# Performance work log

Hardware: AMD Instinct MI355X
Metric: run time of the kernel (lower is better)

## Reference

```python
import jax, jax.numpy as jnp
import numpy as np

EPS = 1e-12  # F.normalize default eps
TEMPERATURE = 1.0


def _l2_normalize(x):
    n = jnp.sqrt(jnp.sum(x * x, axis=-1, keepdims=True))
    return x / jnp.maximum(n, EPS)


def setup_inputs() -> dict:
    key = jax.random.key(0)
    k1, k2 = jax.random.split(key)
    B, C, H, W = 16, 256, 128, 256
    K = 19
    features = jax.random.normal(k1, (B, C, H, W), dtype=jnp.float32)
    prototypes = jax.random.normal(k2, (K, C), dtype=jnp.float32)
    distance_scale = jnp.ones((1,), dtype=jnp.float32)
    return {"features": features, "prototypes": prototypes,
            "distance_scale": distance_scale}


def reference(features, prototypes, distance_scale):
    B, C, H, W = features.shape
    K = prototypes.shape[0]
    # [B,C,H,W] -> [B*H*W, C]
    x = features.transpose(0, 2, 3, 1).reshape(-1, C)
    xn = _l2_normalize(x)            # [N, C]
    pn = _l2_normalize(prototypes)   # [K, C]
    # pairwise Euclidean distance via the stable quadratic expansion
    # ||a-b||^2 = ||a||^2 + ||b||^2 - 2 a.b  (norms ~1 after normalization)
    xx = jnp.sum(xn * xn, axis=-1)   # [N]
    pp = jnp.sum(pn * pn, axis=-1)   # [K]
    d2 = xx[:, None] + pp[None, :] - 2.0 * jnp.einsum('nc,kc->nk', xn, pn)
    dist = jnp.sqrt(jnp.maximum(d2, 0.0))  # [N, K]
    dist = jnp.abs(distance_scale) * dist
    logits = -dist.reshape(B, H, W, K).transpose(0, 3, 1, 2)  # [B,K,H,W]
    return logits / TEMPERATURE
```

## Files before the change

### kernel.cpp

```cpp
#include <hip/hip_runtime.h>


namespace {
constexpr int kC   = 256;
constexpr int kK   = 19;
constexpr int kKP  = 20;
constexpr int kHW  = 128 * 256;
constexpr int kBlock = 256;
constexpr int kPixPerThread = 4;
}

__global__ __launch_bounds__(kBlock, 2)
void isomax_dist_kernel(const float* __restrict__ feat,
                        const float* __restrict__ proto,
                        const float* __restrict__ dscale,
                        float* __restrict__ out)
{
    __shared__ float pn_s[kC * kKP];
    __shared__ float pp_s[kK];

    const int tid  = threadIdx.x;
    const int lane = tid & 63;
    const int wv   = tid >> 6;

    for (int k = wv; k < kK; k += 4) {
        float v[4];
        float ss = 0.f;
        #pragma unroll
        for (int j = 0; j < 4; ++j) {
            v[j] = proto[k * kC + j * 64 + lane];
            ss = fmaf(v[j], v[j], ss);
        }
        #pragma unroll
        for (int m = 1; m < 64; m <<= 1)
            ss += __shfl_xor(ss, m, 64);
        const float nrm = sqrtf(ss);
        const float inv = 1.0f / fmaxf(nrm, 1e-12f);
        #pragma unroll
        for (int j = 0; j < 4; ++j)
            pn_s[(j * 64 + lane) * kKP + k] = v[j] * inv;
        if (lane == 0) pp_s[k] = ss * inv * inv;
    }
    __syncthreads();

    const int gpix = (blockIdx.x * kBlock + tid) * kPixPerThread;
    const int b    = gpix >> 15;
    const int hw   = gpix & (kHW - 1);
    const float* fp = feat + (size_t)b * kC * kHW + hw;

    float xx[4] = {0.f, 0.f, 0.f, 0.f};
    float4 dot[kK];
    #pragma unroll
    for (int k = 0; k < kK; ++k) dot[k] = make_float4(0.f, 0.f, 0.f, 0.f);

    for (int cc = 0; cc < kC; cc += 4) {
        float4 v[4];
        #pragma unroll
        for (int u = 0; u < 4; ++u)
            v[u] = *(const float4*)(fp + (size_t)(cc + u) * kHW);
        #pragma unroll
        for (int u = 0; u < 4; ++u) {
            const int c = cc + u;
            float4 P[5];
            const float4* row = (const float4*)(pn_s + c * kKP);
            #pragma unroll
            for (int q = 0; q < 5; ++q) P[q] = row[q];
            const float* p = (const float*)P;
            xx[0] = fmaf(v[u].x, v[u].x, xx[0]);
            xx[1] = fmaf(v[u].y, v[u].y, xx[1]);
            xx[2] = fmaf(v[u].z, v[u].z, xx[2]);
            xx[3] = fmaf(v[u].w, v[u].w, xx[3]);
            #pragma unroll
            for (int k = 0; k < kK; ++k) {
                dot[k].x = fmaf(p[k], v[u].x, dot[k].x);
                dot[k].y = fmaf(p[k], v[u].y, dot[k].y);
                dot[k].z = fmaf(p[k], v[u].z, dot[k].z);
                dot[k].w = fmaf(p[k], v[u].w, dot[k].w);
            }
        }
    }

    float inv[4], xnsq[4];
    #pragma unroll
    for (int j = 0; j < 4; ++j) {
        const float nrm = sqrtf(xx[j]);
        inv[j]  = 1.0f / fmaxf(nrm, 1e-12f);
        xnsq[j] = xx[j] * inv[j] * inv[j];
    }
    const float sc = fabsf(dscale[0]);

    float* op = out + (size_t)b * kK * kHW + hw;
    #pragma unroll
    for (int k = 0; k < kK; ++k) {
        const float ppk = pp_s[k];
        float4 o;
        o.x = -sc * sqrtf(fmaxf(xnsq[0] + ppk - 2.0f * dot[k].x * inv[0], 0.f));
        o.y = -sc * sqrtf(fmaxf(xnsq[1] + ppk - 2.0f * dot[k].y * inv[1], 0.f));
        o.z = -sc * sqrtf(fmaxf(xnsq[2] + ppk - 2.0f * dot[k].z * inv[2], 0.f));
        o.w = -sc * sqrtf(fmaxf(xnsq[3] + ppk - 2.0f * dot[k].w * inv[3], 0.f));
        *(float4*)(op + (size_t)k * kHW) = o;
    }
}

extern "C" void kernel_launch(void* const* d_in, const int* in_sizes, int n_in,
                              void* d_out, int out_size, void* d_ws, size_t ws_size,
                              hipStream_t stream) {
    const float* feat   = (const float*)d_in[0];
    const float* proto  = (const float*)d_in[1];
    const float* dscale = (const float*)d_in[2];
    float* out = (float*)d_out;

    const int npix    = in_sizes[0] / kC;
    const int threads = npix / kPixPerThread;
    const dim3 grid(threads / kBlock);
    isomax_dist_kernel<<<grid, kBlock, 0, stream>>>(feat, proto, dscale, out);
}
```

Before: 689.2 us.

## Precompute normalized prototypes in workspace and read via scalar constant loads

Prototype normalization moves into a separate single-block kernel that writes the padded normalized table and squared norms to workspace. The main kernel then reads prototype weights through address_space(4) constant pointers, which lets the compiler use scalar loads instead of per-block LDS staging and LDS reads. Pixels per thread drop from 4 to 2 and launch bounds rise to 4 blocks per SIMD, trading register reuse for occupancy. This adds an extra kernel launch and makes every thread issue its own uniform scalar loads of prototype data.

```diff
diff --git a/kernel.cpp b/kernel.cpp
--- a/kernel.cpp
+++ b/kernel.cpp
@@ -1,24 +1,23 @@
 #include <hip/hip_runtime.h>
+#include <stdint.h>
 
 
 namespace {
-constexpr int kC   = 256;
-constexpr int kK   = 19;
-constexpr int kKP  = 20;
-constexpr int kHW  = 128 * 256;
+constexpr int kC     = 256;
+constexpr int kK     = 19;
+constexpr int kKP    = 20;
+constexpr int kHW    = 128 * 256;
 constexpr int kBlock = 256;
-constexpr int kPixPerThread = 4;
+constexpr int kPix   = 2;
 }
 
-__global__ __launch_bounds__(kBlock, 2)
-void isomax_dist_kernel(const float* __restrict__ feat,
-                        const float* __restrict__ proto,
-                        const float* __restrict__ dscale,
-                        float* __restrict__ out)
+typedef __attribute__((address_space(4))) const float* cfp;
+
+__global__ void proto_prep(const float* __restrict__ proto,
+                           float* __restrict__ ws)
 {
-    __shared__ float pn_s[kC * kKP];
-    __shared__ float pp_s[kK];
-
+    float* pw = ws;
+    float* pp = ws + kC * kKP;
     const int tid  = threadIdx.x;
     const int lane = tid & 63;
     const int wv   = tid >> 6;
@@ -34,84 +33,90 @@
         #pragma unroll
         for (int m = 1; m < 64; m <<= 1)
             ss += __shfl_xor(ss, m, 64);
-        const float nrm = sqrtf(ss);
-        const float inv = 1.0f / fmaxf(nrm, 1e-12f);
+        const float inv = 1.0f / fmaxf(sqrtf(ss), 1e-12f);
         #pragma unroll
         for (int j = 0; j < 4; ++j)
-            pn_s[(j * 64 + lane) * kKP + k] = v[j] * inv;
-        if (lane == 0) pp_s[k] = ss * inv * inv;
+            pw[(j * 64 + lane) * kKP + k] = v[j] * inv;
+        if (lane == 0) pp[k] = ss * inv * inv;
     }
-    __syncthreads();
+    pw[tid * kKP + (kKP - 1)] = 0.f;
+}
 
-    const int gpix = (blockIdx.x * kBlock + tid) * kPixPerThread;
+__global__ __launch_bounds__(kBlock, 4)
+void isomax_main(const float* __restrict__ feat,
+                 const float* __restrict__ ws,
+                 const float* __restrict__ dscale,
+                 float* __restrict__ out)
+{
+    const int tid  = threadIdx.x;
+    const int gpix = (blockIdx.x * kBlock + tid) * kPix;
     const int b    = gpix >> 15;
     const int hw   = gpix & (kHW - 1);
-    const float* fp = feat + (size_t)b * kC * kHW + hw;
 
-    float xx[4] = {0.f, 0.f, 0.f, 0.f};
-    float4 dot[kK];
+    const float2* __restrict__ fp =
+        (const float2*)(feat + (size_t)b * kC * kHW + hw);
+
+    cfp pw = (cfp)(uintptr_t)ws;
+
+    float2 xx = make_float2(0.f, 0.f);
+    float2 dot[kK];
     #pragma unroll
-    for (int k = 0; k < kK; ++k) dot[k] = make_float4(0.f, 0.f, 0.f, 0.f);
+    for (int k = 0; k < kK; ++k) dot[k] = make_float2(0.f, 0.f);
 
     for (int cc = 0; cc < kC; cc += 4) {
-        float4 v[4];
+        float2 v[4];
         #pragma unroll
         for (int u = 0; u < 4; ++u)
-            v[u] = *(const float4*)(fp + (size_t)(cc + u) * kHW);
+            v[u] = fp[(size_t)(cc + u) * (kHW / 2)];
         #pragma unroll
         for (int u = 0; u < 4; ++u) {
             const int c = cc + u;
-            float4 P[5];
-            const float4* row = (const float4*)(pn_s + c * kKP);
+            float p[kKP];
             #pragma unroll
-            for (int q = 0; q < 5; ++q) P[q] = row[q];
-            const float* p = (const float*)P;
-            xx[0] = fmaf(v[u].x, v[u].x, xx[0]);
-            xx[1] = fmaf(v[u].y, v[u].y, xx[1]);
-            xx[2] = fmaf(v[u].z, v[u].z, xx[2]);
-            xx[3] = fmaf(v[u].w, v[u].w, xx[3]);
+            for (int q = 0; q < kKP; ++q)
+                p[q] = pw[c * kKP + q];
+            xx.x = fmaf(v[u].x, v[u].x, xx.x);
+            xx.y = fmaf(v[u].y, v[u].y, xx.y);
             #pragma unroll
             for (int k = 0; k < kK; ++k) {
                 dot[k].x = fmaf(p[k], v[u].x, dot[k].x);
                 dot[k].y = fmaf(p[k], v[u].y, dot[k].y);
-                dot[k].z = fmaf(p[k], v[u].z, dot[k].z);
-                dot[k].w = fmaf(p[k], v[u].w, dot[k].w);
             }
         }
     }
 
-    float inv[4], xnsq[4];
-    #pragma unroll
-    for (int j = 0; j < 4; ++j) {
-        const float nrm = sqrtf(xx[j]);
-        inv[j]  = 1.0f / fmaxf(nrm, 1e-12f);
-        xnsq[j] = xx[j] * inv[j] * inv[j];
-    }
-    const float sc = fabsf(dscale[0]);
+    const float ix  = 1.0f / fmaxf(sqrtf(xx.x), 1e-12f);
+    const float iy  = 1.0f / fmaxf(sqrtf(xx.y), 1e-12f);
+    const float xnx = xx.x * ix * ix;
+    const float xny = xx.y * iy * iy;
+    const float sc  = fabsf(dscale[0]);
 
-    float* op = out + (size_t)b * kK * kHW + hw;
+    cfp pp = (cfp)(uintptr_t)(ws + kC * kKP);
+
+    float2* op = (float2*)(out + (size_t)b * kK * kHW + hw);
     #pragma unroll
     for (int k = 0; k < kK; ++k) {
-        const float ppk = pp_s[k];
-        float4 o;
-        o.x = -sc * sqrtf(fmaxf(xnsq[0] + ppk - 2.0f * dot[k].x * inv[0], 0.f));
-        o.y = -sc * sqrtf(fmaxf(xnsq[1] + ppk - 2.0f * dot[k].y * inv[1], 0.f));
-        o.z = -sc * sqrtf(fmaxf(xnsq[2] + ppk - 2.0f * dot[k].z * inv[2], 0.f));
-        o.w = -sc * sqrtf(fmaxf(xnsq[3] + ppk - 2.0f * dot[k].w * inv[3], 0.f));
-        *(float4*)(op + (size_t)k * kHW) = o;
+        const float ppk = pp[k];
+        float2 o;
+        o.x = -sc * sqrtf(fmaxf(xnx + ppk - 2.0f * dot[k].x * ix, 0.f));
+        o.y = -sc * sqrtf(fmaxf(xny + ppk - 2.0f * dot[k].y * iy, 0.f));
+        op[(size_t)k * (kHW / 2)] = o;
     }
 }
 
 extern "C" void kernel_launch(void* const* d_in, const int* in_sizes, int n_in,
                               void* d_out, int out_size, void* d_ws, size_t ws_size,
-                              hipStream_t stream) {
+                              hipStream_t stream)
+{
     const float* feat   = (const float*)d_in[0];
     const float* proto  = (const float*)d_in[1];
     const float* dscale = (const float*)d_in[2];
     float* out = (float*)d_out;
+    float* ws  = (float*)d_ws;
 
-    const int npix    = in_sizes[0] / kC;
-    const int threads = npix / kPixPerThread;
-    const dim3 grid(threads / kBlock);
-    isomax_dist_kernel<<<grid, kBlock, 0, stream>>>(feat, proto, dscale, out);
+    proto_prep<<<dim3(1), dim3(kBlock), 0, stream>>>(proto, ws);
+
+    const int npix = in_sizes[0] / kC;
+    const dim3 grid(npix / (kBlock * kPix));
+    isomax_main<<<grid, dim3(kBlock), 0, stream>>>(feat, ws, dscale, out);
 }
```

Result: no change. 695.6 us (+0.9%).
